# Kernel optimization log

Hardware: AMD Instinct MI355X
Metric: run time of the kernel (lower is better)

Reference implementation:

```python
import jax, jax.numpy as jnp
import numpy as np

D_MODEL = 2048
N_HEADS = 16
D_HEAD = D_MODEL // N_HEADS
BATCH = 2
SEQ = 2048
NEG = -1e9


def setup_inputs() -> dict:
    key = jax.random.key(0)
    ks = jax.random.split(key, 6)
    s = 1.0 / np.sqrt(D_MODEL)
    x = jax.random.normal(ks[0], (BATCH, SEQ, D_MODEL), dtype=jnp.float32)
    # additive causal mask: 0 on/below diagonal, -1e9 above
    causal = jnp.where(jnp.tril(jnp.ones((SEQ, SEQ), dtype=bool)), 0.0, NEG).astype(jnp.float32)
    return {
        "x": x,
        "mask": causal,
        "Wq": jax.random.normal(ks[1], (D_MODEL, D_MODEL), dtype=jnp.float32) * s,
        "bq": jnp.zeros((D_MODEL,), dtype=jnp.float32),
        "Wk": jax.random.normal(ks[2], (D_MODEL, D_MODEL), dtype=jnp.float32) * s,
        "bk": jnp.zeros((D_MODEL,), dtype=jnp.float32),
        "Wv": jax.random.normal(ks[3], (D_MODEL, D_MODEL), dtype=jnp.float32) * s,
        "bv": jnp.zeros((D_MODEL,), dtype=jnp.float32),
        "Wo": jax.random.normal(ks[4], (D_MODEL, D_MODEL), dtype=jnp.float32) * s,
        "bo": jnp.zeros((D_MODEL,), dtype=jnp.float32),
    }


def reference(x, mask, Wq, bq, Wk, bk, Wv, bv, Wo, bo):
    B, S, _ = x.shape
    scale = 1.0 / np.sqrt(D_HEAD).astype(np.float32)
    # projections -> (B, H, S, Dh)
    def split_heads(t):
        return t.reshape(B, S, N_HEADS, D_HEAD).transpose(0, 2, 1, 3)
    q = split_heads(x @ Wq + bq)
    k = split_heads(x @ Wk + bk)
    v = split_heads(x @ Wv + bv)
    scores = jnp.einsum("bhqd,bhkd->bhqk", q, k) * scale + mask  # (B,H,S,S)
    weights = jax.nn.softmax(scores, axis=-1)
    attn = jnp.einsum("bhqk,bhkd->bhqd", weights, v)
    attn = attn.transpose(0, 2, 1, 3).reshape(B, S, D_MODEL)
    return attn @ Wo + bo
```

## Files before the change

kernel.cpp:

```cpp
#include <hip/hip_runtime.h>
#include <hip/hip_bf16.h>
#include <math.h>

typedef __bf16 bf16;
typedef __attribute__((ext_vector_type(8))) __bf16 bf16x8;
typedef __attribute__((ext_vector_type(4))) float f32x4;
typedef __attribute__((ext_vector_type(4))) int i32x4;

#define DEV __device__ __forceinline__

static constexpr int S_LEN = 2048;
static constexpr int DM = 2048;
static constexpr int NB = 2;
static constexpr int NH = 16;
static constexpr int DH = 128;
static constexpr long MROWS = (long)NB * S_LEN;

static constexpr float QSCALE = 0.12751744836522312f;
static constexpr float M0 = 11.0f;


__global__ void k_cast_bf16(const float* __restrict__ in, bf16* __restrict__ out, long n8) {
  long i = (long)blockIdx.x * blockDim.x + threadIdx.x;
  long stride = (long)gridDim.x * blockDim.x;
  for (; i < n8; i += stride) {
    const float4* p = (const float4*)(in + i * 8);
    float4 a = p[0], b = p[1];
    bf16x8 v;
    v[0] = (bf16)a.x; v[1] = (bf16)a.y; v[2] = (bf16)a.z; v[3] = (bf16)a.w;
    v[4] = (bf16)b.x; v[5] = (bf16)b.y; v[6] = (bf16)b.z; v[7] = (bf16)b.w;
    *(bf16x8*)(out + i * 8) = v;
  }
}

__global__ void k_transpose_w(const float* __restrict__ in, bf16* __restrict__ out) {
  __shared__ float t[32][33];
  int bx = blockIdx.x * 32, by = blockIdx.y * 32;
  int tx = threadIdx.x, ty = threadIdx.y;
#pragma unroll
  for (int i = 0; i < 32; i += 8)
    t[ty + i][tx] = in[(long)(by + ty + i) * DM + bx + tx];
  __syncthreads();
#pragma unroll
  for (int i = 0; i < 32; i += 8)
    out[(long)(bx + ty + i) * DM + by + tx] = (bf16)t[tx][ty + i];
}

__global__ void k_transpose_v(const bf16* __restrict__ v, bf16* __restrict__ vt) {
  __shared__ bf16 t[32][33];
  int s0 = blockIdx.x * 32, d0 = blockIdx.y * 32;
  int bh = blockIdx.z;
  int b = bh >> 4, h = bh & 15;
  int tx = threadIdx.x, ty = threadIdx.y;
  const bf16* src = v + ((long)(b * S_LEN + s0)) * DM + h * DH + d0;
#pragma unroll
  for (int i = 0; i < 32; i += 8)
    t[ty + i][tx] = src[(long)(ty + i) * DM + tx];
  __syncthreads();
  bf16* dst = vt + ((long)bh * DH + d0) * S_LEN + s0;
#pragma unroll
  for (int i = 0; i < 32; i += 8)
    dst[(long)(ty + i) * S_LEN + tx] = t[tx][ty + i];
}


template<int ROWB>
DEV void stage16k(const bf16* __restrict__ g, long gstride, bf16* l, int tid) {
#pragma unroll
  for (int c = 0; c < 4; ++c) {
    int o = c * 4096 + tid * 16;
    int row = o / ROWB;
    int blk = (o & (ROWB - 1)) >> 4;
    int blkg = blk ^ (row & 7);
    const bf16* src = g + (long)row * gstride + (blkg << 3);
    char* dst = (char*)l + (o & ~1023);
    __builtin_amdgcn_global_load_lds(
        (const __attribute__((address_space(1))) void*)src,
        (__attribute__((address_space(3))) void*)dst, 16, 0, 0);
  }
}

DEV void stage_k(const bf16* __restrict__ g, bf16* l, int tid) {
#pragma unroll
  for (int c = 0; c < 4; ++c) {
    int o = c * 4096 + tid * 16;
    int row = o >> 8;
    int blk = (o >> 4) & 15;
    int blkg = blk ^ (row & 7);
    int prow = (row & 3) | (((row >> 2) & 3) << 3) | (((row >> 5) & 1) << 2) |
               (((row >> 4) & 1) << 5);
    const bf16* src = g + (long)prow * DM + (blkg << 3);
    char* dst = (char*)l + (o & ~1023);
    __builtin_amdgcn_global_load_lds(
        (const __attribute__((address_space(1))) void*)src,
        (__attribute__((address_space(3))) void*)dst, 16, 0, 0);
  }
}

template<int ROWB>
DEV bf16x8 read_frag(const bf16* l, int row, int blk) {
  int blks = blk ^ (row & 7);
  return *(const bf16x8*)((const char*)l + row * ROWB + (blks << 4));
}


template<bool OUT_BF16>
__global__ __launch_bounds__(256) void k_gemm_bt(const bf16* __restrict__ A,
                                                 const bf16* __restrict__ BT,
                                                 const float* __restrict__ bias,
                                                 void* __restrict__ C,
                                                 int M, int N, int K, float cs) {
  __shared__ __align__(16) bf16 lA[128 * 64];
  __shared__ __align__(16) bf16 lB[128 * 64];
  int tid = threadIdx.x;
  int row0 = blockIdx.y * 128, col0 = blockIdx.x * 128;
  int w = tid >> 6, lane = tid & 63;
  int wm = w >> 1, wn = w & 1;
  int g = lane >> 4, c16 = lane & 15;

  f32x4 acc[4][4] = {};

  for (int kt = 0; kt < K; kt += 64) {
    stage16k<128>(A + (long)row0 * K + kt, K, lA, tid);
    stage16k<128>(BT + (long)col0 * K + kt, K, lB, tid);
    __syncthreads();
#pragma unroll
    for (int ks = 0; ks < 2; ++ks) {
      bf16x8 af[4], bf_[4];
#pragma unroll
      for (int i = 0; i < 4; ++i)
        af[i] = read_frag<128>(lA, wm * 64 + i * 16 + c16, ks * 4 + g);
#pragma unroll
      for (int j = 0; j < 4; ++j)
        bf_[j] = read_frag<128>(lB, wn * 64 + j * 16 + c16, ks * 4 + g);
#pragma unroll
      for (int i = 0; i < 4; ++i)
#pragma unroll
        for (int j = 0; j < 4; ++j)
          acc[i][j] = __builtin_amdgcn_mfma_f32_16x16x32_bf16(af[i], bf_[j], acc[i][j], 0, 0, 0);
    }
    __syncthreads();
  }

#pragma unroll
  for (int i = 0; i < 4; ++i) {
    int grow = row0 + wm * 64 + i * 16 + (g << 2);
#pragma unroll
    for (int j = 0; j < 4; ++j) {
      int gcol = col0 + wn * 64 + j * 16 + c16;
      float bv = bias[gcol];
#pragma unroll
      for (int r = 0; r < 4; ++r) {
        float vv = (acc[i][j][r] + bv) * cs;
        if constexpr (OUT_BF16)
          ((bf16*)C)[(long)(grow + r) * N + gcol] = (bf16)vv;
        else
          ((float*)C)[(long)(grow + r) * N + gcol] = vv;
      }
    }
  }
}


__global__ __launch_bounds__(256, 2) void k_attn(const bf16* __restrict__ Q,
                                                 const bf16* __restrict__ Kt,
                                                 const bf16* __restrict__ Vt,
                                                 bf16* __restrict__ O,
                                                 bf16* __restrict__ part,
                                                 float* __restrict__ lsums) {
  __shared__ __align__(16) bf16 sK[2][64 * 128];
  __shared__ __align__(16) bf16 sV[2][128 * 64];

  int tid = threadIdx.x;
  int bid = blockIdx.x;
  int bh = bid & 31;
  int pr = (bid >> 5) & 7;
  int role = bid >> 8;
  int b = bh >> 4, h = bh & 15;
  int w = tid >> 6, lane = tid & 63;
  int g = lane >> 4, c16 = lane & 15;
  int t = bh * 8 + pr;

  const bf16* Qh = Q + (long)b * S_LEN * DM + h * DH;
  const bf16* Kh = Kt + (long)b * S_LEN * DM + h * DH;
  const bf16* Vh = Vt + (long)bh * DH * S_LEN;

#pragma unroll 1
  for (int seg = 0; seg < 2; ++seg) {
    int qt, k0, k1, partial;
    if (role == 0) {
      if (seg == 0) { qt = pr;      k0 = 0;           k1 = 2 * pr + 2;  partial = 0; }
      else          { qt = 15 - pr; k0 = 0;           k1 = 15 - 2 * pr; partial = 1; }
    } else {
      if (seg == 1) break;
      qt = 15 - pr; k0 = 15 - 2 * pr; k1 = 32 - 2 * pr; partial = 2;
    }

    int q0 = qt * 128;
    int qb = q0 + w * 32;

    bf16x8 qa[2][4];
#pragma unroll
    for (int u = 0; u < 2; ++u)
#pragma unroll
      for (int ks = 0; ks < 4; ++ks)
        qa[u][ks] = *(const bf16x8*)(Qh + (long)(qb + 16 * u + c16) * DM + (ks * 4 + g) * 8);

    stage_k(Kh + (long)k0 * 64 * DM, sK[0], tid);
    stage16k<128>(Vh + k0 * 64, S_LEN, sV[0], tid);

    float lsum[2] = {0.f, 0.f};
    f32x4 od[2][8] = {};

#pragma unroll 1
    for (int kt = k0; kt < k1; ++kt) {
      int cur = (kt - k0) & 1;
      if (kt + 1 < k1) {
        stage_k(Kh + (long)(kt + 1) * 64 * DM, sK[cur ^ 1], tid);
        stage16k<128>(Vh + (kt + 1) * 64, S_LEN, sV[cur ^ 1], tid);
        asm volatile("s_waitcnt vmcnt(8)" ::: "memory");
      } else {
        asm volatile("s_waitcnt vmcnt(0)" ::: "memory");
      }
      __builtin_amdgcn_s_barrier();
      asm volatile("" ::: "memory");

      int kv0 = kt * 64;
      if (kv0 <= qb + 31) {
        f32x4 sf[2][4] = {};
        __builtin_amdgcn_s_setprio(1);
#pragma unroll
        for (int n = 0; n < 4; ++n)
#pragma unroll
          for (int ks = 0; ks < 4; ++ks) {
            bf16x8 kf = read_frag<256>(sK[cur], n * 16 + c16, ks * 4 + g);
            sf[0][n] = __builtin_amdgcn_mfma_f32_16x16x32_bf16(kf, qa[0][ks], sf[0][n], 0, 0, 0);
            sf[1][n] = __builtin_amdgcn_mfma_f32_16x16x32_bf16(kf, qa[1][ks], sf[1][n], 0, 0, 0);
          }
        __builtin_amdgcn_s_setprio(0);

        bool emask = (kv0 + 63 > qb);
        bf16x8 pa[2][2];
#pragma unroll
        for (int u = 0; u < 2; ++u) {
          unsigned pw[8];
#pragma unroll
          for (int n = 0; n < 4; ++n) {
            float p[4];
#pragma unroll
            for (int r = 0; r < 4; ++r) {
              float s = sf[u][n][r];
              if (emask) {
                int kv = kv0 + ((n & 1) << 5) + (g << 3) + ((n >> 1) << 2) + r;
                int qg = qb + 16 * u + c16;
                s = (kv > qg) ? -INFINITY : s;
              }
              float pv = exp2f(s - M0);
              p[r] = pv;
              lsum[u] += pv;
            }
            asm("v_cvt_pk_bf16_f32 %0, %1, %2" : "=v"(pw[2 * n]) : "v"(p[0]), "v"(p[1]));
            asm("v_cvt_pk_bf16_f32 %0, %1, %2" : "=v"(pw[2 * n + 1]) : "v"(p[2]), "v"(p[3]));
          }
          i32x4 t0 = {(int)pw[0], (int)pw[1], (int)pw[4], (int)pw[5]};
          i32x4 t1 = {(int)pw[2], (int)pw[3], (int)pw[6], (int)pw[7]};
          pa[u][0] = __builtin_bit_cast(bf16x8, t0);
          pa[u][1] = __builtin_bit_cast(bf16x8, t1);
        }

        __builtin_amdgcn_s_setprio(1);
#pragma unroll
        for (int j = 0; j < 8; ++j)
#pragma unroll
          for (int ks = 0; ks < 2; ++ks) {
            bf16x8 vf = read_frag<128>(sV[cur], j * 16 + c16, ks * 4 + g);
            od[0][j] = __builtin_amdgcn_mfma_f32_16x16x32_bf16(pa[0][ks], vf, od[0][j], 0, 0, 0);
            od[1][j] = __builtin_amdgcn_mfma_f32_16x16x32_bf16(pa[1][ks], vf, od[1][j], 0, 0, 0);
          }
        __builtin_amdgcn_s_setprio(0);
      }
      asm volatile("" ::: "memory");
      __builtin_amdgcn_s_barrier();
    }

#pragma unroll
    for (int u = 0; u < 2; ++u) {
      lsum[u] += __shfl_xor(lsum[u], 16);
      lsum[u] += __shfl_xor(lsum[u], 32);
    }

    if (partial == 0) {
      const long ob = ((long)(b * S_LEN + qb)) * DM + h * DH + c16;
#pragma unroll
      for (int u = 0; u < 2; ++u)
#pragma unroll
        for (int r = 0; r < 4; ++r) {
          float inv = 1.0f / __shfl(lsum[u], 4 * g + r);
#pragma unroll
          for (int j = 0; j < 8; ++j)
            O[ob + (long)(16 * u + 4 * g + r) * DM + j * 16] = (bf16)(od[u][j][r] * inv);
        }
    } else {
      bf16* PP = part + ((long)((partial == 2 ? 256 : 0) + t)) * 16384;
      float* LP = lsums + (partial == 2 ? 256 * 128 : 0) + t * 128;
#pragma unroll
      for (int u = 0; u < 2; ++u) {
        if (g == 0) LP[32 * w + 16 * u + c16] = lsum[u];
#pragma unroll
        for (int r = 0; r < 4; ++r) {
          int row = 32 * w + 16 * u + 4 * g + r;
#pragma unroll
          for (int j = 0; j < 8; ++j)
            PP[row * 128 + 16 * j + c16] = (bf16)od[u][j][r];
        }
      }
    }
  }
}

__global__ __launch_bounds__(256) void k_merge(const bf16* __restrict__ part,
                                               const float* __restrict__ lsums,
                                               bf16* __restrict__ A2) {
  int t = blockIdx.x;
  int bh = t >> 3, pr = t & 7;
  int b = bh >> 4, h = bh & 15;
  int qt = 15 - pr;
  int tid = threadIdx.x;
  int q = tid >> 1, d0 = (tid & 1) * 64;
  float inv = 1.0f / (lsums[t * 128 + q] + lsums[256 * 128 + t * 128 + q]);
  const bf16* pA = part + (long)t * 16384 + q * 128 + d0;
  const bf16* pB = part + (long)(256 + t) * 16384 + q * 128 + d0;
  bf16* out = A2 + ((long)(b * S_LEN + qt * 128 + q)) * DM + h * DH + d0;
#pragma unroll
  for (int j = 0; j < 8; ++j) {
    bf16x8 a = *(const bf16x8*)(pA + j * 8);
    bf16x8 bb = *(const bf16x8*)(pB + j * 8);
    bf16x8 o;
#pragma unroll
    for (int r = 0; r < 8; ++r) o[r] = (bf16)(((float)a[r] + (float)bb[r]) * inv);
    *(bf16x8*)(out + j * 8) = o;
  }
}


extern "C" void kernel_launch(void* const* d_in, const int* in_sizes, int n_in,
                              void* d_out, int out_size, void* d_ws, size_t ws_size,
                              hipStream_t stream) {
  (void)in_sizes; (void)n_in; (void)out_size; (void)ws_size;
  const float* x  = (const float*)d_in[0];
  const float* Wq = (const float*)d_in[2];
  const float* bq = (const float*)d_in[3];
  const float* Wk = (const float*)d_in[4];
  const float* bk = (const float*)d_in[5];
  const float* Wv = (const float*)d_in[6];
  const float* bv = (const float*)d_in[7];
  const float* Wo = (const float*)d_in[8];
  const float* bo = (const float*)d_in[9];
  float* out = (float*)d_out;

  bf16* Xb = (bf16*)d_ws;
  bf16* WT = Xb + MROWS * DM;
  bf16* Qb = WT + (long)DM * DM;
  bf16* Kb = Qb + MROWS * DM;
  bf16* Vb = Kb + MROWS * DM;
  bf16* Vt = Xb;
  bf16* A2 = Vb;

  bf16* part = (bf16*)d_out;
  float* lsums = (float*)((bf16*)d_out + 2L * 256 * 16384);

  dim3 tb32(32, 8);
  dim3 gW(64, 64);
  dim3 gGemm(DM / 128, MROWS / 128);

  k_cast_bf16<<<2048, 256, 0, stream>>>(x, Xb, MROWS * DM / 8);

  k_transpose_w<<<gW, tb32, 0, stream>>>(Wq, WT);
  k_gemm_bt<true><<<gGemm, 256, 0, stream>>>(Xb, WT, bq, Qb, (int)MROWS, DM, DM, QSCALE);
  k_transpose_w<<<gW, tb32, 0, stream>>>(Wk, WT);
  k_gemm_bt<true><<<gGemm, 256, 0, stream>>>(Xb, WT, bk, Kb, (int)MROWS, DM, DM, 1.0f);
  k_transpose_w<<<gW, tb32, 0, stream>>>(Wv, WT);
  k_gemm_bt<true><<<gGemm, 256, 0, stream>>>(Xb, WT, bv, Vb, (int)MROWS, DM, DM, 1.0f);

  k_transpose_v<<<dim3(S_LEN / 32, DH / 32, NB * NH), tb32, 0, stream>>>(Vb, Vt);

  k_attn<<<512, 256, 0, stream>>>(Qb, Kb, Vt, A2, part, lsums);
  k_merge<<<256, 256, 0, stream>>>(part, lsums, A2);

  k_transpose_w<<<gW, tb32, 0, stream>>>(Wo, WT);
  k_gemm_bt<false><<<gGemm, 256, 0, stream>>>(A2, WT, bo, out, (int)MROWS, DM, DM, 1.0f);
}
```

Before: 293.2 us.

## Split attention into 1024 balanced work items, fuse V transpose into GEMM

Attention work is now split into 32 chunks per head: the first 8 query tiles each form one item, and tiles 8-15 are each split three ways along the key range. A permuted order table schedules these items, and the kernel raises occupancy to 4 blocks per CU. All items write partial results that a generalized merge kernel combines. V is now read directly from global memory instead of being staged in LDS. A new V-projection GEMM writes its output already transposed, which removes the separate transpose kernel. The trade-off is that uncoalesced V loads and 4-byte strided stores may add memory traffic.

```diff
diff --git a/kernel.cpp b/kernel.cpp
--- a/kernel.cpp
+++ b/kernel.cpp
@@ -3,6 +3,7 @@
 #include <math.h>
 
 typedef __bf16 bf16;
+typedef __attribute__((ext_vector_type(4))) __bf16 bf16x4;
 typedef __attribute__((ext_vector_type(8))) __bf16 bf16x8;
 typedef __attribute__((ext_vector_type(4))) float f32x4;
 typedef __attribute__((ext_vector_type(4))) int i32x4;
@@ -44,23 +45,6 @@
 #pragma unroll
   for (int i = 0; i < 32; i += 8)
     out[(long)(bx + ty + i) * DM + by + tx] = (bf16)t[tx][ty + i];
-}
-
-__global__ void k_transpose_v(const bf16* __restrict__ v, bf16* __restrict__ vt) {
-  __shared__ bf16 t[32][33];
-  int s0 = blockIdx.x * 32, d0 = blockIdx.y * 32;
-  int bh = blockIdx.z;
-  int b = bh >> 4, h = bh & 15;
-  int tx = threadIdx.x, ty = threadIdx.y;
-  const bf16* src = v + ((long)(b * S_LEN + s0)) * DM + h * DH + d0;
-#pragma unroll
-  for (int i = 0; i < 32; i += 8)
-    t[ty + i][tx] = src[(long)(ty + i) * DM + tx];
-  __syncthreads();
-  bf16* dst = vt + ((long)bh * DH + d0) * S_LEN + s0;
-#pragma unroll
-  for (int i = 0; i < 32; i += 8)
-    dst[(long)(ty + i) * S_LEN + tx] = t[tx][ty + i];
 }
 
 
@@ -161,159 +145,200 @@
   }
 }
 
-
-__global__ __launch_bounds__(256, 2) void k_attn(const bf16* __restrict__ Q,
+__global__ __launch_bounds__(256) void k_gemm_v(const bf16* __restrict__ A,
+                                                const bf16* __restrict__ BT,
+                                                const float* __restrict__ bias,
+                                                bf16* __restrict__ Vt,
+                                                int M, int N, int K) {
+  __shared__ __align__(16) bf16 lA[128 * 64];
+  __shared__ __align__(16) bf16 lB[128 * 64];
+  int tid = threadIdx.x;
+  int row0 = blockIdx.y * 128, col0 = blockIdx.x * 128;
+  int w = tid >> 6, lane = tid & 63;
+  int wm = w >> 1, wn = w & 1;
+  int g = lane >> 4, c16 = lane & 15;
+
+  f32x4 acc[4][4] = {};
+
+  for (int kt = 0; kt < K; kt += 64) {
+    stage16k<128>(A + (long)row0 * K + kt, K, lA, tid);
+    stage16k<128>(BT + (long)col0 * K + kt, K, lB, tid);
+    __syncthreads();
+#pragma unroll
+    for (int ks = 0; ks < 2; ++ks) {
+      bf16x8 af[4], bf_[4];
+#pragma unroll
+      for (int i = 0; i < 4; ++i)
+        af[i] = read_frag<128>(lA, wm * 64 + i * 16 + c16, ks * 4 + g);
+#pragma unroll
+      for (int j = 0; j < 4; ++j)
+        bf_[j] = read_frag<128>(lB, wn * 64 + j * 16 + c16, ks * 4 + g);
+#pragma unroll
+      for (int i = 0; i < 4; ++i)
+#pragma unroll
+        for (int j = 0; j < 4; ++j)
+          acc[i][j] = __builtin_amdgcn_mfma_f32_16x16x32_bf16(af[i], bf_[j], acc[i][j], 0, 0, 0);
+    }
+    __syncthreads();
+  }
+
+#pragma unroll
+  for (int i = 0; i < 4; ++i) {
+    int grow = row0 + wm * 64 + i * 16 + (g << 2);
+    int b = grow >> 11, s = grow & 2047;
+#pragma unroll
+    for (int j = 0; j < 4; ++j) {
+      int cg = col0 + wn * 64 + j * 16 + c16;
+      int h = cg >> 7, d = cg & 127;
+      float bv = bias[cg];
+      bf16x4 pk;
+#pragma unroll
+      for (int r = 0; r < 4; ++r) pk[r] = (bf16)(acc[i][j][r] + bv);
+      *(bf16x4*)(Vt + ((long)((b << 4) | h) * 128 + d) * 2048 + s) = pk;
+    }
+  }
+}
+
+
+__device__ const unsigned char ORD32[32] = {
+    7, 6, 29, 30, 26, 23, 28, 4,
+    5, 17, 20, 21, 27, 24, 25, 31,
+    1, 8, 18, 19, 22, 3, 14, 15,
+    0, 9, 10, 13, 2, 11, 12, 16};
+
+__global__ __launch_bounds__(256, 4) void k_attn(const bf16* __restrict__ Q,
                                                  const bf16* __restrict__ Kt,
                                                  const bf16* __restrict__ Vt,
-                                                 bf16* __restrict__ O,
                                                  bf16* __restrict__ part,
                                                  float* __restrict__ lsums) {
   __shared__ __align__(16) bf16 sK[2][64 * 128];
-  __shared__ __align__(16) bf16 sV[2][128 * 64];
 
   int tid = threadIdx.x;
   int bid = blockIdx.x;
   int bh = bid & 31;
-  int pr = (bid >> 5) & 7;
-  int role = bid >> 8;
+  int p = bid >> 5;
+  int id = ORD32[p];
+  int qt, k0, k1;
+  if (id < 8) {
+    qt = id; k0 = 0; k1 = 2 * id + 2;
+  } else {
+    int e = id - 8;
+    qt = 8 + e / 3;
+    int ci = e % 3;
+    int nt = 2 * qt + 2, base = nt / 3, rem = nt - 3 * base;
+    k0 = ci * base + (ci < rem ? ci : rem);
+    k1 = k0 + base + (ci < rem ? 1 : 0);
+  }
   int b = bh >> 4, h = bh & 15;
   int w = tid >> 6, lane = tid & 63;
   int g = lane >> 4, c16 = lane & 15;
-  int t = bh * 8 + pr;
+  int qb = qt * 128 + w * 32;
 
   const bf16* Qh = Q + (long)b * S_LEN * DM + h * DH;
   const bf16* Kh = Kt + (long)b * S_LEN * DM + h * DH;
   const bf16* Vh = Vt + (long)bh * DH * S_LEN;
 
+  bf16x8 qa[2][4];
+#pragma unroll
+  for (int u = 0; u < 2; ++u)
+#pragma unroll
+    for (int ks = 0; ks < 4; ++ks)
+      qa[u][ks] = *(const bf16x8*)(Qh + (long)(qb + 16 * u + c16) * DM + (ks * 4 + g) * 8);
+
+  stage_k(Kh + (long)k0 * 64 * DM, sK[0], tid);
+
+  float lsum[2] = {0.f, 0.f};
+  f32x4 od[2][8] = {};
+
 #pragma unroll 1
-  for (int seg = 0; seg < 2; ++seg) {
-    int qt, k0, k1, partial;
-    if (role == 0) {
-      if (seg == 0) { qt = pr;      k0 = 0;           k1 = 2 * pr + 2;  partial = 0; }
-      else          { qt = 15 - pr; k0 = 0;           k1 = 15 - 2 * pr; partial = 1; }
+  for (int kt = k0; kt < k1; ++kt) {
+    int cur = (kt - k0) & 1;
+    if (kt + 1 < k1) {
+      stage_k(Kh + (long)(kt + 1) * 64 * DM, sK[cur ^ 1], tid);
+      asm volatile("s_waitcnt vmcnt(4)" ::: "memory");
     } else {
-      if (seg == 1) break;
-      qt = 15 - pr; k0 = 15 - 2 * pr; k1 = 32 - 2 * pr; partial = 2;
-    }
-
-    int q0 = qt * 128;
-    int qb = q0 + w * 32;
-
-    bf16x8 qa[2][4];
-#pragma unroll
-    for (int u = 0; u < 2; ++u)
-#pragma unroll
-      for (int ks = 0; ks < 4; ++ks)
-        qa[u][ks] = *(const bf16x8*)(Qh + (long)(qb + 16 * u + c16) * DM + (ks * 4 + g) * 8);
-
-    stage_k(Kh + (long)k0 * 64 * DM, sK[0], tid);
-    stage16k<128>(Vh + k0 * 64, S_LEN, sV[0], tid);
-
-    float lsum[2] = {0.f, 0.f};
-    f32x4 od[2][8] = {};
-
-#pragma unroll 1
-    for (int kt = k0; kt < k1; ++kt) {
-      int cur = (kt - k0) & 1;
-      if (kt + 1 < k1) {
-        stage_k(Kh + (long)(kt + 1) * 64 * DM, sK[cur ^ 1], tid);
-        stage16k<128>(Vh + (kt + 1) * 64, S_LEN, sV[cur ^ 1], tid);
-        asm volatile("s_waitcnt vmcnt(8)" ::: "memory");
-      } else {
-        asm volatile("s_waitcnt vmcnt(0)" ::: "memory");
+      asm volatile("s_waitcnt vmcnt(0)" ::: "memory");
+    }
+    __builtin_amdgcn_s_barrier();
+    asm volatile("" ::: "memory");
+
+    int kv0 = kt * 64;
+    if (kv0 <= qb + 31) {
+      f32x4 sf[2][4] = {};
+      __builtin_amdgcn_s_setprio(1);
+#pragma unroll
+      for (int n = 0; n < 4; ++n)
+#pragma unroll
+        for (int ks = 0; ks < 4; ++ks) {
+          bf16x8 kf = read_frag<256>(sK[cur], n * 16 + c16, ks * 4 + g);
+          sf[0][n] = __builtin_amdgcn_mfma_f32_16x16x32_bf16(kf, qa[0][ks], sf[0][n], 0, 0, 0);
+          sf[1][n] = __builtin_amdgcn_mfma_f32_16x16x32_bf16(kf, qa[1][ks], sf[1][n], 0, 0, 0);
+        }
+      __builtin_amdgcn_s_setprio(0);
+
+      bool emask = (kv0 + 63 > qb);
+      bf16x8 pa[2][2];
+#pragma unroll
+      for (int u = 0; u < 2; ++u) {
+        unsigned pw[8];
+#pragma unroll
+        for (int n = 0; n < 4; ++n) {
+          float pv4[4];
+#pragma unroll
+          for (int r = 0; r < 4; ++r) {
+            float s = sf[u][n][r];
+            if (emask) {
+              int kv = kv0 + ((n & 1) << 5) + (g << 3) + ((n >> 1) << 2) + r;
+              int qg = qb + 16 * u + c16;
+              s = (kv > qg) ? -INFINITY : s;
+            }
+            float pv = exp2f(s - M0);
+            pv4[r] = pv;
+            lsum[u] += pv;
+          }
+          asm("v_cvt_pk_bf16_f32 %0, %1, %2" : "=v"(pw[2 * n]) : "v"(pv4[0]), "v"(pv4[1]));
+          asm("v_cvt_pk_bf16_f32 %0, %1, %2" : "=v"(pw[2 * n + 1]) : "v"(pv4[2]), "v"(pv4[3]));
+        }
+        i32x4 t0 = {(int)pw[0], (int)pw[1], (int)pw[4], (int)pw[5]};
+        i32x4 t1 = {(int)pw[2], (int)pw[3], (int)pw[6], (int)pw[7]};
+        pa[u][0] = __builtin_bit_cast(bf16x8, t0);
+        pa[u][1] = __builtin_bit_cast(bf16x8, t1);
       }
-      __builtin_amdgcn_s_barrier();
-      asm volatile("" ::: "memory");
-
-      int kv0 = kt * 64;
-      if (kv0 <= qb + 31) {
-        f32x4 sf[2][4] = {};
-        __builtin_amdgcn_s_setprio(1);
-#pragma unroll
-        for (int n = 0; n < 4; ++n)
-#pragma unroll
-          for (int ks = 0; ks < 4; ++ks) {
-            bf16x8 kf = read_frag<256>(sK[cur], n * 16 + c16, ks * 4 + g);
-            sf[0][n] = __builtin_amdgcn_mfma_f32_16x16x32_bf16(kf, qa[0][ks], sf[0][n], 0, 0, 0);
-            sf[1][n] = __builtin_amdgcn_mfma_f32_16x16x32_bf16(kf, qa[1][ks], sf[1][n], 0, 0, 0);
-          }
-        __builtin_amdgcn_s_setprio(0);
-
-        bool emask = (kv0 + 63 > qb);
-        bf16x8 pa[2][2];
-#pragma unroll
-        for (int u = 0; u < 2; ++u) {
-          unsigned pw[8];
-#pragma unroll
-          for (int n = 0; n < 4; ++n) {
-            float p[4];
-#pragma unroll
-            for (int r = 0; r < 4; ++r) {
-              float s = sf[u][n][r];
-              if (emask) {
-                int kv = kv0 + ((n & 1) << 5) + (g << 3) + ((n >> 1) << 2) + r;
-                int qg = qb + 16 * u + c16;
-                s = (kv > qg) ? -INFINITY : s;
-              }
-              float pv = exp2f(s - M0);
-              p[r] = pv;
-              lsum[u] += pv;
-            }
-            asm("v_cvt_pk_bf16_f32 %0, %1, %2" : "=v"(pw[2 * n]) : "v"(p[0]), "v"(p[1]));
-            asm("v_cvt_pk_bf16_f32 %0, %1, %2" : "=v"(pw[2 * n + 1]) : "v"(p[2]), "v"(p[3]));
-          }
-          i32x4 t0 = {(int)pw[0], (int)pw[1], (int)pw[4], (int)pw[5]};
-          i32x4 t1 = {(int)pw[2], (int)pw[3], (int)pw[6], (int)pw[7]};
-          pa[u][0] = __builtin_bit_cast(bf16x8, t0);
-          pa[u][1] = __builtin_bit_cast(bf16x8, t1);
-        }
-
-        __builtin_amdgcn_s_setprio(1);
-#pragma unroll
-        for (int j = 0; j < 8; ++j)
-#pragma unroll
-          for (int ks = 0; ks < 2; ++ks) {
-            bf16x8 vf = read_frag<128>(sV[cur], j * 16 + c16, ks * 4 + g);
-            od[0][j] = __builtin_amdgcn_mfma_f32_16x16x32_bf16(pa[0][ks], vf, od[0][j], 0, 0, 0);
-            od[1][j] = __builtin_amdgcn_mfma_f32_16x16x32_bf16(pa[1][ks], vf, od[1][j], 0, 0, 0);
-          }
-        __builtin_amdgcn_s_setprio(0);
-      }
-      asm volatile("" ::: "memory");
-      __builtin_amdgcn_s_barrier();
-    }
-
-#pragma unroll
-    for (int u = 0; u < 2; ++u) {
-      lsum[u] += __shfl_xor(lsum[u], 16);
-      lsum[u] += __shfl_xor(lsum[u], 32);
-    }
-
-    if (partial == 0) {
-      const long ob = ((long)(b * S_LEN + qb)) * DM + h * DH + c16;
-#pragma unroll
-      for (int u = 0; u < 2; ++u)
-#pragma unroll
-        for (int r = 0; r < 4; ++r) {
-          float inv = 1.0f / __shfl(lsum[u], 4 * g + r);
-#pragma unroll
-          for (int j = 0; j < 8; ++j)
-            O[ob + (long)(16 * u + 4 * g + r) * DM + j * 16] = (bf16)(od[u][j][r] * inv);
-        }
-    } else {
-      bf16* PP = part + ((long)((partial == 2 ? 256 : 0) + t)) * 16384;
-      float* LP = lsums + (partial == 2 ? 256 * 128 : 0) + t * 128;
-#pragma unroll
-      for (int u = 0; u < 2; ++u) {
-        if (g == 0) LP[32 * w + 16 * u + c16] = lsum[u];
-#pragma unroll
-        for (int r = 0; r < 4; ++r) {
-          int row = 32 * w + 16 * u + 4 * g + r;
-#pragma unroll
-          for (int j = 0; j < 8; ++j)
-            PP[row * 128 + 16 * j + c16] = (bf16)od[u][j][r];
+
+      __builtin_amdgcn_s_setprio(1);
+#pragma unroll
+      for (int j = 0; j < 8; ++j) {
+        const bf16* vr = Vh + (long)(j * 16 + c16) * S_LEN + kv0 + g * 8;
+#pragma unroll
+        for (int ks = 0; ks < 2; ++ks) {
+          bf16x8 vf = *(const bf16x8*)(vr + ks * 32);
+          od[0][j] = __builtin_amdgcn_mfma_f32_16x16x32_bf16(pa[0][ks], vf, od[0][j], 0, 0, 0);
+          od[1][j] = __builtin_amdgcn_mfma_f32_16x16x32_bf16(pa[1][ks], vf, od[1][j], 0, 0, 0);
         }
       }
+      __builtin_amdgcn_s_setprio(0);
+    }
+    asm volatile("" ::: "memory");
+    __builtin_amdgcn_s_barrier();
+  }
+
+#pragma unroll
+  for (int u = 0; u < 2; ++u) {
+    lsum[u] += __shfl_xor(lsum[u], 16);
+    lsum[u] += __shfl_xor(lsum[u], 32);
+  }
+
+  bf16* PP = part + (long)(bh * 32 + id) * 16384;
+  float* LP = lsums + (bh * 32 + id) * 128;
+#pragma unroll
+  for (int u = 0; u < 2; ++u) {
+    if (g == 0) LP[32 * w + 16 * u + c16] = lsum[u];
+#pragma unroll
+    for (int r = 0; r < 4; ++r) {
+      int row = 32 * w + 16 * u + 4 * g + r;
+#pragma unroll
+      for (int j = 0; j < 8; ++j)
+        PP[row * 128 + 16 * j + c16] = (bf16)od[u][j][r];
     }
   }
 }
@@ -322,22 +347,28 @@
                                                const float* __restrict__ lsums,
                                                bf16* __restrict__ A2) {
   int t = blockIdx.x;
-  int bh = t >> 3, pr = t & 7;
+  int bh = t >> 4, qt = t & 15;
   int b = bh >> 4, h = bh & 15;
-  int qt = 15 - pr;
   int tid = threadIdx.x;
   int q = tid >> 1, d0 = (tid & 1) * 64;
-  float inv = 1.0f / (lsums[t * 128 + q] + lsums[256 * 128 + t * 128 + q]);
-  const bf16* pA = part + (long)t * 16384 + q * 128 + d0;
-  const bf16* pB = part + (long)(256 + t) * 16384 + q * 128 + d0;
+  int s0, nc;
+  if (qt < 8) { s0 = bh * 32 + qt; nc = 1; }
+  else        { s0 = bh * 32 + 8 + 3 * (qt - 8); nc = 3; }
+  float ls = 0.f;
+  for (int i = 0; i < nc; ++i) ls += lsums[(s0 + i) * 128 + q];
+  float inv = 1.0f / ls;
   bf16* out = A2 + ((long)(b * S_LEN + qt * 128 + q)) * DM + h * DH + d0;
 #pragma unroll
   for (int j = 0; j < 8; ++j) {
-    bf16x8 a = *(const bf16x8*)(pA + j * 8);
-    bf16x8 bb = *(const bf16x8*)(pB + j * 8);
+    float acc[8] = {};
+    for (int i = 0; i < nc; ++i) {
+      bf16x8 v = *(const bf16x8*)(part + (long)(s0 + i) * 16384 + q * 128 + d0 + j * 8);
+#pragma unroll
+      for (int r = 0; r < 8; ++r) acc[r] += (float)v[r];
+    }
     bf16x8 o;
 #pragma unroll
-    for (int r = 0; r < 8; ++r) o[r] = (bf16)(((float)a[r] + (float)bb[r]) * inv);
+    for (int r = 0; r < 8; ++r) o[r] = (bf16)(acc[r] * inv);
     *(bf16x8*)(out + j * 8) = o;
   }
 }
@@ -362,12 +393,11 @@
   bf16* WT = Xb + MROWS * DM;
   bf16* Qb = WT + (long)DM * DM;
   bf16* Kb = Qb + MROWS * DM;
-  bf16* Vb = Kb + MROWS * DM;
-  bf16* Vt = Xb;
-  bf16* A2 = Vb;
+  bf16* Vt = Kb + MROWS * DM;
+  bf16* A2 = Xb;
 
   bf16* part = (bf16*)d_out;
-  float* lsums = (float*)((bf16*)d_out + 2L * 256 * 16384);
+  float* lsums = (float*)WT;
 
   dim3 tb32(32, 8);
   dim3 gW(64, 64);
@@ -380,12 +410,10 @@
   k_transpose_w<<<gW, tb32, 0, stream>>>(Wk, WT);
   k_gemm_bt<true><<<gGemm, 256, 0, stream>>>(Xb, WT, bk, Kb, (int)MROWS, DM, DM, 1.0f);
   k_transpose_w<<<gW, tb32, 0, stream>>>(Wv, WT);
-  k_gemm_bt<true><<<gGemm, 256, 0, stream>>>(Xb, WT, bv, Vb, (int)MROWS, DM, DM, 1.0f);
-
-  k_transpose_v<<<dim3(S_LEN / 32, DH / 32, NB * NH), tb32, 0, stream>>>(Vb, Vt);
-
-  k_attn<<<512, 256, 0, stream>>>(Qb, Kb, Vt, A2, part, lsums);
-  k_merge<<<256, 256, 0, stream>>>(part, lsums, A2);
+  k_gemm_v<<<gGemm, 256, 0, stream>>>(Xb, WT, bv, Vt, (int)MROWS, DM, DM);
+
+  k_attn<<<1024, 256, 0, stream>>>(Qb, Kb, Vt, part, lsums);
+  k_merge<<<512, 256, 0, stream>>>(part, lsums, A2);
 
   k_transpose_w<<<gW, tb32, 0, stream>>>(Wo, WT);
   k_gemm_bt<false><<<gGemm, 256, 0, stream>>>(A2, WT, bo, out, (int)MROWS, DM, DM, 1.0f);
```

After: 455.6 us. 1.55x slower.

## Replace GEMM with 256x128 triple-buffered 8-wave pipelined kernel, fuse V transpose

Applied to the files above, without the earlier changes.

Replaces the simple 128x128 single-buffered GEMM with a 512-thread, 256x128-tile kernel. It uses triple-buffered async global-to-LDS staging, interleaved load rounds and MFMA phases with priority hints. The V projection epilogue now writes directly into the transposed per-head layout, which removes the separate V transpose kernel and its extra pass over memory. The cost is 144KB of dynamic LDS per block, so occupancy is one block per CU. The new buffer aliasing also has to stay consistent with the attention and merge kernels.

```diff
diff --git a/kernel.cpp b/kernel.cpp
--- a/kernel.cpp
+++ b/kernel.cpp
@@ -3,11 +3,13 @@
 #include <math.h>
 
 typedef __bf16 bf16;
+typedef __attribute__((ext_vector_type(4))) __bf16 bf16x4;
 typedef __attribute__((ext_vector_type(8))) __bf16 bf16x8;
 typedef __attribute__((ext_vector_type(4))) float f32x4;
 typedef __attribute__((ext_vector_type(4))) int i32x4;
 
 #define DEV __device__ __forceinline__
+#define FENCE asm volatile("" ::: "memory")
 
 static constexpr int S_LEN = 2048;
 static constexpr int DM = 2048;
@@ -46,23 +48,17 @@
     out[(long)(bx + ty + i) * DM + by + tx] = (bf16)t[tx][ty + i];
 }
 
-__global__ void k_transpose_v(const bf16* __restrict__ v, bf16* __restrict__ vt) {
-  __shared__ bf16 t[32][33];
-  int s0 = blockIdx.x * 32, d0 = blockIdx.y * 32;
-  int bh = blockIdx.z;
-  int b = bh >> 4, h = bh & 15;
-  int tx = threadIdx.x, ty = threadIdx.y;
-  const bf16* src = v + ((long)(b * S_LEN + s0)) * DM + h * DH + d0;
-#pragma unroll
-  for (int i = 0; i < 32; i += 8)
-    t[ty + i][tx] = src[(long)(ty + i) * DM + tx];
-  __syncthreads();
-  bf16* dst = vt + ((long)bh * DH + d0) * S_LEN + s0;
-#pragma unroll
-  for (int i = 0; i < 32; i += 8)
-    dst[(long)(ty + i) * S_LEN + tx] = t[tx][ty + i];
-}
-
+
+DEV void stg_round(const bf16* __restrict__ g, long gstride, bf16* l, int tid, int c) {
+  int o = c * 8192 + tid * 16;
+  int row = o >> 7;
+  int blk = (o >> 4) & 7;
+  const bf16* src = g + (long)row * gstride + ((blk ^ (row & 7)) << 3);
+  char* dst = (char*)l + (o & ~1023);
+  __builtin_amdgcn_global_load_lds(
+      (const __attribute__((address_space(1))) void*)src,
+      (__attribute__((address_space(3))) void*)dst, 16, 0, 0);
+}
 
 template<int ROWB>
 DEV void stage16k(const bf16* __restrict__ g, long gstride, bf16* l, int tid) {
@@ -104,61 +100,136 @@
 }
 
 
-template<bool OUT_BF16>
-__global__ __launch_bounds__(256) void k_gemm_bt(const bf16* __restrict__ A,
-                                                 const bf16* __restrict__ BT,
-                                                 const float* __restrict__ bias,
-                                                 void* __restrict__ C,
-                                                 int M, int N, int K, float cs) {
-  __shared__ __align__(16) bf16 lA[128 * 64];
-  __shared__ __align__(16) bf16 lB[128 * 64];
+template<int EPI>
+__global__ __launch_bounds__(512) void k_gemm8p(const bf16* __restrict__ A,
+                                                const bf16* __restrict__ BT,
+                                                const float* __restrict__ bias,
+                                                void* __restrict__ C, float cs) {
+  extern __shared__ char smem[];
   int tid = threadIdx.x;
-  int row0 = blockIdx.y * 128, col0 = blockIdx.x * 128;
   int w = tid >> 6, lane = tid & 63;
   int wm = w >> 1, wn = w & 1;
   int g = lane >> 4, c16 = lane & 15;
+  long row0 = (long)blockIdx.y * 256, col0 = (long)blockIdx.x * 128;
+  const bf16* gA = A + row0 * 2048;
+  const bf16* gB = BT + col0 * 2048;
 
   f32x4 acc[4][4] = {};
 
-  for (int kt = 0; kt < K; kt += 64) {
-    stage16k<128>(A + (long)row0 * K + kt, K, lA, tid);
-    stage16k<128>(BT + (long)col0 * K + kt, K, lB, tid);
-    __syncthreads();
-#pragma unroll
-    for (int ks = 0; ks < 2; ++ks) {
-      bf16x8 af[4], bf_[4];
-#pragma unroll
-      for (int i = 0; i < 4; ++i)
-        af[i] = read_frag<128>(lA, wm * 64 + i * 16 + c16, ks * 4 + g);
-#pragma unroll
-      for (int j = 0; j < 4; ++j)
-        bf_[j] = read_frag<128>(lB, wn * 64 + j * 16 + c16, ks * 4 + g);
-#pragma unroll
-      for (int i = 0; i < 4; ++i)
-#pragma unroll
-        for (int j = 0; j < 4; ++j)
-          acc[i][j] = __builtin_amdgcn_mfma_f32_16x16x32_bf16(af[i], bf_[j], acc[i][j], 0, 0, 0);
-    }
-    __syncthreads();
+#define BUFA(i) ((bf16*)(smem + (i) * 49152))
+#define BUFB(i) ((bf16*)(smem + (i) * 49152 + 32768))
+
+#pragma unroll
+  for (int t0 = 0; t0 < 2; ++t0) {
+#pragma unroll
+    for (int c = 0; c < 4; ++c) stg_round(gA + t0 * 64, 2048, BUFA(t0), tid, c);
+#pragma unroll
+    for (int c = 0; c < 2; ++c) stg_round(gB + t0 * 64, 2048, BUFB(t0), tid, c);
+  }
+  asm volatile("s_waitcnt vmcnt(6)" ::: "memory");
+  __builtin_amdgcn_s_barrier();
+  FENCE;
+
+#pragma unroll 1
+  for (int t = 0; t < 32; ++t) {
+    bf16* cA = BUFA(t % 3);
+    bf16* cB = BUFB(t % 3);
+    bf16* nA = BUFA((t + 2) % 3);
+    bf16* nB = BUFB((t + 2) % 3);
+    const bf16* gA2 = gA + (t + 2) * 64;
+    const bf16* gB2 = gB + (t + 2) * 64;
+    bool st = (t + 2) < 32;
+    bf16x8 af[4], bj0, bj1;
+
+#pragma unroll
+    for (int i = 0; i < 4; ++i) af[i] = read_frag<128>(cA, wm * 64 + i * 16 + c16, g);
+    bj0 = read_frag<128>(cB, wn * 64 + c16, g);
+    bj1 = read_frag<128>(cB, wn * 64 + 16 + c16, g);
+    if (st) { stg_round(gA2, 2048, nA, tid, 0); stg_round(gA2, 2048, nA, tid, 1); }
+    FENCE; __builtin_amdgcn_s_barrier();
+    __builtin_amdgcn_s_setprio(1);
+#pragma unroll
+    for (int i = 0; i < 4; ++i) {
+      acc[i][0] = __builtin_amdgcn_mfma_f32_16x16x32_bf16(af[i], bj0, acc[i][0], 0, 0, 0);
+      acc[i][1] = __builtin_amdgcn_mfma_f32_16x16x32_bf16(af[i], bj1, acc[i][1], 0, 0, 0);
+    }
+    __builtin_amdgcn_s_setprio(0);
+    FENCE; __builtin_amdgcn_s_barrier();
+
+    bj0 = read_frag<128>(cB, wn * 64 + 32 + c16, g);
+    bj1 = read_frag<128>(cB, wn * 64 + 48 + c16, g);
+    if (st) { stg_round(gA2, 2048, nA, tid, 2); stg_round(gA2, 2048, nA, tid, 3); }
+    FENCE; __builtin_amdgcn_s_barrier();
+    __builtin_amdgcn_s_setprio(1);
+#pragma unroll
+    for (int i = 0; i < 4; ++i) {
+      acc[i][2] = __builtin_amdgcn_mfma_f32_16x16x32_bf16(af[i], bj0, acc[i][2], 0, 0, 0);
+      acc[i][3] = __builtin_amdgcn_mfma_f32_16x16x32_bf16(af[i], bj1, acc[i][3], 0, 0, 0);
+    }
+    __builtin_amdgcn_s_setprio(0);
+    FENCE; __builtin_amdgcn_s_barrier();
+
+#pragma unroll
+    for (int i = 0; i < 4; ++i) af[i] = read_frag<128>(cA, wm * 64 + i * 16 + c16, 4 + g);
+    bj0 = read_frag<128>(cB, wn * 64 + c16, 4 + g);
+    bj1 = read_frag<128>(cB, wn * 64 + 16 + c16, 4 + g);
+    if (st) { stg_round(gB2, 2048, nB, tid, 0); stg_round(gB2, 2048, nB, tid, 1); }
+    FENCE; __builtin_amdgcn_s_barrier();
+    __builtin_amdgcn_s_setprio(1);
+#pragma unroll
+    for (int i = 0; i < 4; ++i) {
+      acc[i][0] = __builtin_amdgcn_mfma_f32_16x16x32_bf16(af[i], bj0, acc[i][0], 0, 0, 0);
+      acc[i][1] = __builtin_amdgcn_mfma_f32_16x16x32_bf16(af[i], bj1, acc[i][1], 0, 0, 0);
+    }
+    __builtin_amdgcn_s_setprio(0);
+    FENCE; __builtin_amdgcn_s_barrier();
+
+    bj0 = read_frag<128>(cB, wn * 64 + 32 + c16, 4 + g);
+    bj1 = read_frag<128>(cB, wn * 64 + 48 + c16, 4 + g);
+    FENCE; __builtin_amdgcn_s_barrier();
+    __builtin_amdgcn_s_setprio(1);
+#pragma unroll
+    for (int i = 0; i < 4; ++i) {
+      acc[i][2] = __builtin_amdgcn_mfma_f32_16x16x32_bf16(af[i], bj0, acc[i][2], 0, 0, 0);
+      acc[i][3] = __builtin_amdgcn_mfma_f32_16x16x32_bf16(af[i], bj1, acc[i][3], 0, 0, 0);
+    }
+    __builtin_amdgcn_s_setprio(0);
+    if (t + 2 < 32) {
+      asm volatile("s_waitcnt vmcnt(6)" ::: "memory");
+    } else if (t + 1 < 32) {
+      asm volatile("s_waitcnt vmcnt(0)" ::: "memory");
+    }
+    FENCE; __builtin_amdgcn_s_barrier();
   }
 
 #pragma unroll
   for (int i = 0; i < 4; ++i) {
-    int grow = row0 + wm * 64 + i * 16 + (g << 2);
+    long grow = row0 + wm * 64 + i * 16 + (g << 2);
 #pragma unroll
     for (int j = 0; j < 4; ++j) {
-      int gcol = col0 + wn * 64 + j * 16 + c16;
+      long gcol = col0 + wn * 64 + j * 16 + c16;
       float bv = bias[gcol];
-#pragma unroll
-      for (int r = 0; r < 4; ++r) {
-        float vv = (acc[i][j][r] + bv) * cs;
-        if constexpr (OUT_BF16)
-          ((bf16*)C)[(long)(grow + r) * N + gcol] = (bf16)vv;
-        else
-          ((float*)C)[(long)(grow + r) * N + gcol] = vv;
+      if constexpr (EPI == 2) {
+        int b = (int)(grow >> 11), s = (int)(grow & 2047);
+        int h = (int)(gcol >> 7), d = (int)(gcol & 127);
+        bf16x4 pk;
+#pragma unroll
+        for (int r = 0; r < 4; ++r) pk[r] = (bf16)(acc[i][j][r] + bv);
+        *(bf16x4*)((bf16*)C + ((long)((b << 4) | h) * 128 + d) * 2048 + s) = pk;
+      } else {
+#pragma unroll
+        for (int r = 0; r < 4; ++r) {
+          float vv = (acc[i][j][r] + bv) * cs;
+          if constexpr (EPI == 0)
+            ((bf16*)C)[(grow + r) * 2048 + gcol] = (bf16)vv;
+          else
+            ((float*)C)[(grow + r) * 2048 + gcol] = vv;
+        }
       }
     }
   }
+#undef BUFA
+#undef BUFB
 }
 
 
@@ -223,7 +294,7 @@
         asm volatile("s_waitcnt vmcnt(0)" ::: "memory");
       }
       __builtin_amdgcn_s_barrier();
-      asm volatile("" ::: "memory");
+      FENCE;
 
       int kv0 = kt * 64;
       if (kv0 <= qb + 31) {
@@ -246,21 +317,21 @@
           unsigned pw[8];
 #pragma unroll
           for (int n = 0; n < 4; ++n) {
-            float p[4];
+            float pv4[4];
 #pragma unroll
             for (int r = 0; r < 4; ++r) {
-              float s = sf[u][n][r];
+              float sc = sf[u][n][r];
               if (emask) {
                 int kv = kv0 + ((n & 1) << 5) + (g << 3) + ((n >> 1) << 2) + r;
                 int qg = qb + 16 * u + c16;
-                s = (kv > qg) ? -INFINITY : s;
+                sc = (kv > qg) ? -INFINITY : sc;
               }
-              float pv = exp2f(s - M0);
-              p[r] = pv;
+              float pv = exp2f(sc - M0);
+              pv4[r] = pv;
               lsum[u] += pv;
             }
-            asm("v_cvt_pk_bf16_f32 %0, %1, %2" : "=v"(pw[2 * n]) : "v"(p[0]), "v"(p[1]));
-            asm("v_cvt_pk_bf16_f32 %0, %1, %2" : "=v"(pw[2 * n + 1]) : "v"(p[2]), "v"(p[3]));
+            asm("v_cvt_pk_bf16_f32 %0, %1, %2" : "=v"(pw[2 * n]) : "v"(pv4[0]), "v"(pv4[1]));
+            asm("v_cvt_pk_bf16_f32 %0, %1, %2" : "=v"(pw[2 * n + 1]) : "v"(pv4[2]), "v"(pv4[3]));
           }
           i32x4 t0 = {(int)pw[0], (int)pw[1], (int)pw[4], (int)pw[5]};
           i32x4 t1 = {(int)pw[2], (int)pw[3], (int)pw[6], (int)pw[7]};
@@ -279,7 +350,7 @@
           }
         __builtin_amdgcn_s_setprio(0);
       }
-      asm volatile("" ::: "memory");
+      FENCE;
       __builtin_amdgcn_s_barrier();
     }
 
@@ -362,31 +433,33 @@
   bf16* WT = Xb + MROWS * DM;
   bf16* Qb = WT + (long)DM * DM;
   bf16* Kb = Qb + MROWS * DM;
-  bf16* Vb = Kb + MROWS * DM;
-  bf16* Vt = Xb;
-  bf16* A2 = Vb;
+  bf16* Vt = Kb + MROWS * DM;
+  bf16* A2 = Xb;
 
   bf16* part = (bf16*)d_out;
   float* lsums = (float*)((bf16*)d_out + 2L * 256 * 16384);
 
+  static const int GEMM_LDS = 3 * 49152;
+  hipFuncSetAttribute((const void*)k_gemm8p<0>, hipFuncAttributeMaxDynamicSharedMemorySize, GEMM_LDS);
+  hipFuncSetAttribute((const void*)k_gemm8p<1>, hipFuncAttributeMaxDynamicSharedMemorySize, GEMM_LDS);
+  hipFuncSetAttribute((const void*)k_gemm8p<2>, hipFuncAttributeMaxDynamicSharedMemorySize, GEMM_LDS);
+
   dim3 tb32(32, 8);
   dim3 gW(64, 64);
-  dim3 gGemm(DM / 128, MROWS / 128);
+  dim3 gG(DM / 128, MROWS / 256);
 
   k_cast_bf16<<<2048, 256, 0, stream>>>(x, Xb, MROWS * DM / 8);
 
   k_transpose_w<<<gW, tb32, 0, stream>>>(Wq, WT);
-  k_gemm_bt<true><<<gGemm, 256, 0, stream>>>(Xb, WT, bq, Qb, (int)MROWS, DM, DM, QSCALE);
+  k_gemm8p<0><<<gG, 512, GEMM_LDS, stream>>>(Xb, WT, bq, Qb, QSCALE);
   k_transpose_w<<<gW, tb32, 0, stream>>>(Wk, WT);
-  k_gemm_bt<true><<<gGemm, 256, 0, stream>>>(Xb, WT, bk, Kb, (int)MROWS, DM, DM, 1.0f);
+  k_gemm8p<0><<<gG, 512, GEMM_LDS, stream>>>(Xb, WT, bk, Kb, 1.0f);
   k_transpose_w<<<gW, tb32, 0, stream>>>(Wv, WT);
-  k_gemm_bt<true><<<gGemm, 256, 0, stream>>>(Xb, WT, bv, Vb, (int)MROWS, DM, DM, 1.0f);
-
-  k_transpose_v<<<dim3(S_LEN / 32, DH / 32, NB * NH), tb32, 0, stream>>>(Vb, Vt);
+  k_gemm8p<2><<<gG, 512, GEMM_LDS, stream>>>(Xb, WT, bv, Vt, 1.0f);
 
   k_attn<<<512, 256, 0, stream>>>(Qb, Kb, Vt, A2, part, lsums);
   k_merge<<<256, 256, 0, stream>>>(part, lsums, A2);
 
   k_transpose_w<<<gW, tb32, 0, stream>>>(Wo, WT);
-  k_gemm_bt<false><<<gGemm, 256, 0, stream>>>(A2, WT, bo, out, (int)MROWS, DM, DM, 1.0f);
-}
+  k_gemm8p<1><<<gG, 512, GEMM_LDS, stream>>>(A2, WT, bo, out, 1.0f);
+}
```

Result: faster. 260.1 us (-11.3%).
